# Performance work log

Measured on AMD Instinct MI355X. Metric: run time of the kernel, lower is better.

## Reference

```python
import jax, jax.numpy as jnp
import numpy as np

B, V, J, NB = 1024, 3889, 33, 10
P = (J - 1) * 9  # 288 pose-blendshape basis


def setup_inputs() -> dict:
    key = jax.random.key(0)
    ks = jax.random.split(key, 9)
    n = lambda k, s, sc=1.0: jax.random.normal(k, s, dtype=jnp.float32) * sc
    betas = n(ks[0], (B, NB))
    global_orient = n(ks[1], (B, 3), 0.5)
    body_pose = n(ks[2], (B, (J - 1) * 3), 0.3)
    transl = n(ks[3], (B, 3))
    v_template = n(ks[4], (V, 3))
    shapedirs = n(ks[5], (V, 3, NB), 0.01)
    posedirs = n(ks[6], (P, V * 3), 0.01)
    jr = jax.random.uniform(ks[7], (J, V), dtype=jnp.float32)
    J_regressor = jr / jnp.sum(jr, axis=1, keepdims=True)  # rows sum to 1
    w = jax.random.uniform(ks[8], (V, J), dtype=jnp.float32)
    lbs_weights = w / jnp.sum(w, axis=1, keepdims=True)
    # kinematic tree: chain, parents[i] < i; root parent handled specially
    parents = np.maximum(np.arange(J) - 1, 0).astype(np.int64)
    return {"betas": betas, "global_orient": global_orient, "body_pose": body_pose,
            "transl": transl, "v_template": v_template, "shapedirs": shapedirs,
            "posedirs": posedirs, "J_regressor": J_regressor,
            "lbs_weights": lbs_weights, "parents": parents}


def _rodrigues(rot_vecs):
    """Axis-angle [.., 3] -> rotation matrices [.., 3, 3] (Rodrigues)."""
    angle = jnp.linalg.norm(rot_vecs + 1e-8, axis=-1, keepdims=True)
    axis = rot_vecs / angle
    rx, ry, rz = axis[..., 0], axis[..., 1], axis[..., 2]
    z = jnp.zeros_like(rx)
    K = jnp.stack([z, -rz, ry, rz, z, -rx, -ry, rx, z], axis=-1)
    K = K.reshape(rot_vecs.shape[:-1] + (3, 3))
    s = jnp.sin(angle)[..., None]
    c = jnp.cos(angle)[..., None]
    return jnp.eye(3, dtype=rot_vecs.dtype) + s * K + (1.0 - c) * (K @ K)


def _lbs(betas, global_orient, body_pose, transl, v_template, shapedirs,
         posedirs, J_regressor, lbs_weights, parents):
    Bn = betas.shape[0]
    par = np.asarray(parents)  # static kinematic tree
    Jn = par.shape[0]
    # shape blendshapes
    v_shaped = v_template[None] + jnp.einsum('bl,vcl->bvc', betas, shapedirs)
    joints = jnp.einsum('jv,bvc->bjc', J_regressor, v_shaped)  # [B,J,3]
    # pose -> rotation matrices
    full_pose = jnp.concatenate([global_orient, body_pose], axis=1).reshape(Bn, Jn, 3)
    rot = _rodrigues(full_pose)  # [B,J,3,3]
    # pose blendshapes (identity-subtracted, root excluded)
    pose_feat = (rot[:, 1:] - jnp.eye(3, dtype=rot.dtype)).reshape(Bn, -1)  # [B,288]
    v_posed = v_shaped + (pose_feat @ posedirs).reshape(Bn, -1, 3)
    # forward kinematics: compose 4x4 transforms along the tree
    rel = joints.at[:, 1:].add(-joints[:, par[1:]])  # relative joint locations
    Tmat = jnp.concatenate([rot, rel[..., None]], axis=-1)  # [B,J,3,4]
    bottom = jnp.broadcast_to(jnp.array([0., 0., 0., 1.], Tmat.dtype), (Bn, Jn, 1, 4))
    Tmat = jnp.concatenate([Tmat, bottom], axis=2)  # [B,J,4,4]
    chain = [Tmat[:, 0]]
    for i in range(1, Jn):  # fixed small loop over joints
        chain.append(chain[int(par[i])] @ Tmat[:, i])
    transforms = jnp.stack(chain, axis=1)  # [B,J,4,4]
    # remove rest-pose joint locations from the transforms
    jh = jnp.concatenate([joints, jnp.zeros((Bn, Jn, 1), joints.dtype)], axis=-1)[..., None]
    A = transforms - jnp.pad(transforms @ jh, ((0, 0), (0, 0), (0, 0), (3, 0)))
    # linear blend skinning
    T = jnp.einsum('vj,bjmn->bvmn', lbs_weights, A)  # [B,V,4,4]
    vh = jnp.concatenate([v_posed, jnp.ones(v_posed.shape[:-1] + (1,), v_posed.dtype)], axis=-1)
    verts = jnp.einsum('bvmn,bvn->bvm', T, vh)[..., :3]
    return verts + transl[:, None]


def reference(betas, global_orient, body_pose, transl, v_template, shapedirs,
              posedirs, J_regressor, lbs_weights, parents):
    return _lbs(betas, global_orient, body_pose, transl, v_template, shapedirs,
                posedirs, J_regressor, lbs_weights, parents)
```

## Files before the change

### kernel.cpp

```cpp
#include <hip/hip_runtime.h>
#include <math.h>

#define B_  1024
#define V_  3889
#define J_  33
#define NB_ 10
#define P_  288
#define N3  11667
#define NT_ 122
#define NPAD (NT_*96)

typedef short bf16x8 __attribute__((ext_vector_type(8)));
typedef float f32x4  __attribute__((ext_vector_type(4)));

__device__ __forceinline__ unsigned short f2bf(float f) {
  union { float f; unsigned u; } v; v.f = f;
  unsigned r = v.u + 0x7FFFu + ((v.u >> 16) & 1u);
  return (unsigned short)(r >> 16);
}
__device__ __forceinline__ float bf2f(unsigned short h) {
  union { unsigned u; float f; } v; v.u = ((unsigned)h) << 16; return v.f;
}

#define PREP_JS   33
#define PREP_CVT  399
#define PREP_NB   463

__global__ __launch_bounds__(256) void k_prep(
    const float* __restrict__ Jreg, const float* __restrict__ vt,
    const float* __restrict__ sd, const float* __restrict__ pdirs,
    const float* __restrict__ lbsw,
    float* __restrict__ JS, float* __restrict__ bj,
    unsigned short* __restrict__ pdT, unsigned short* __restrict__ wbf)
{
  __shared__ __align__(16) unsigned char su[38016];
  const int bid = blockIdx.x;
  const int t = threadIdx.x;

  if (bid < PREP_JS) {
    float* red = (float*)su;
    const int j = bid;
    if (t < 128) {
      float acc[33];
      #pragma unroll
      for (int e = 0; e < 33; ++e) acc[e] = 0.f;
      for (int v = t; v < V_; v += 128) {
        float r = Jreg[j*V_ + v];
        #pragma unroll
        for (int c = 0; c < 3; ++c) {
          acc[c*11 + 10] += r * vt[v*3 + c];
          #pragma unroll
          for (int l = 0; l < NB_; ++l)
            acc[c*11 + l] += r * sd[v*30 + c*10 + l];
        }
      }
      #pragma unroll
      for (int e = 0; e < 33; ++e) red[e*128 + t] = acc[e];
    }
    __syncthreads();
    if (t < 33) {
      float s = 0.f;
      for (int i = 0; i < 128; ++i) s += red[t*128 + i];
      int c = t / 11, l = t % 11;
      if (l == 10) bj[j*3 + c] = s;
      else         JS[(j*3 + c)*NB_ + l] = s;
    }
  } else if (bid < PREP_CVT) {
    float* tile = (float*)su;
    const int bb = bid - PREP_JS;
    const int nt = bb / 3;
    const int c0 = (bb % 3) * 32;
    for (int i = t; i < P_*32; i += 256) {
      int k = i >> 5, c = i & 31;
      int gc = nt*96 + c0 + c;
      tile[k*33 + c] = (gc < N3) ? pdirs[(size_t)k*N3 + gc] : 0.f;
    }
    __syncthreads();
    for (int o = t; o < 32*P_; o += 256) {
      int c = o / P_, k = o % P_;
      pdT[((size_t)(nt*96 + c0 + c))*P_ + k] = f2bf(tile[k*33 + c]);
    }
  } else {
    const int bb = bid - PREP_CVT;
    const int total = 4096*96;
    for (int i = bb*256 + t; i < total; i += 64*256) {
      int v = i / 96, k = i - 96*v;
      float val = 0.f;
      if (v < V_) {
        if (k < 33) val = lbsw[(size_t)v*33 + k];
        else if (k < 66) {
          float w = lbsw[(size_t)v*33 + (k-33)];
          val = w - bf2f(f2bf(w));
        }
      }
      wbf[i] = f2bf(val);
    }
  }
}

__global__ __launch_bounds__(64) void k_pose(
    const float* __restrict__ betas, const float* __restrict__ go,
    const float* __restrict__ bp, const float* __restrict__ JS,
    const float* __restrict__ bj,
    unsigned short* __restrict__ pfb,
    unsigned short* __restrict__ Abf)
{
  const int b = blockIdx.x;
  const int t = threadIdx.x;
  __shared__ float rot[J_][9];
  __shared__ float jnt[J_][3];
  __shared__ float Ash[J_][12];
  __shared__ float bsh[NB_];
  if (t < NB_) bsh[t] = betas[b*NB_ + t];
  __syncthreads();
  if (t < J_) {
    #pragma unroll
    for (int c = 0; c < 3; ++c) {
      float s = bj[t*3 + c];
      #pragma unroll
      for (int l = 0; l < NB_; ++l) s += bsh[l] * JS[(t*3 + c)*NB_ + l];
      jnt[t][c] = s;
    }
    float px, py, pz;
    if (t == 0) { px = go[b*3+0]; py = go[b*3+1]; pz = go[b*3+2]; }
    else {
      const float* p = bp + (size_t)b*((J_-1)*3) + (t-1)*3;
      px = p[0]; py = p[1]; pz = p[2];
    }
    float ax = px + 1e-8f, ay = py + 1e-8f, az = pz + 1e-8f;
    float ang = sqrtf(ax*ax + ay*ay + az*az);
    float inv = 1.0f / ang;
    float ux = px*inv, uy = py*inv, uz = pz*inv;
    float sn = sinf(ang), cs = cosf(ang);
    float K[9] = {0.f,-uz,uy,  uz,0.f,-ux,  -uy,ux,0.f};
    float R[9];
    #pragma unroll
    for (int r = 0; r < 3; ++r)
      #pragma unroll
      for (int c = 0; c < 3; ++c) {
        float k2 = K[r*3+0]*K[0*3+c] + K[r*3+1]*K[1*3+c] + K[r*3+2]*K[2*3+c];
        float id = (r == c) ? 1.f : 0.f;
        R[r*3+c] = id + sn*K[r*3+c] + (1.f - cs)*k2;
      }
    #pragma unroll
    for (int e = 0; e < 9; ++e) rot[t][e] = R[e];
    if (t >= 1) {
      #pragma unroll
      for (int e = 0; e < 9; ++e)
        pfb[(size_t)b*P_ + (t-1)*9 + e] = f2bf(R[e] - ((e==0||e==4||e==8) ? 1.f : 0.f));
    }
  }
  __syncthreads();
  if (t == 0) {
    float G[12];
    #pragma unroll
    for (int r = 0; r < 3; ++r) {
      G[r*4+0] = rot[0][r*3+0]; G[r*4+1] = rot[0][r*3+1];
      G[r*4+2] = rot[0][r*3+2]; G[r*4+3] = jnt[0][r];
    }
    for (int j = 0; j < J_; ++j) {
      if (j > 0) {
        float rel0 = jnt[j][0] - jnt[j-1][0];
        float rel1 = jnt[j][1] - jnt[j-1][1];
        float rel2 = jnt[j][2] - jnt[j-1][2];
        float N[12];
        #pragma unroll
        for (int r = 0; r < 3; ++r) {
          #pragma unroll
          for (int c = 0; c < 3; ++c)
            N[r*4+c] = G[r*4+0]*rot[j][0*3+c] + G[r*4+1]*rot[j][1*3+c] + G[r*4+2]*rot[j][2*3+c];
          N[r*4+3] = G[r*4+0]*rel0 + G[r*4+1]*rel1 + G[r*4+2]*rel2 + G[r*4+3];
        }
        #pragma unroll
        for (int e = 0; e < 12; ++e) G[e] = N[e];
      }
      #pragma unroll
      for (int r = 0; r < 3; ++r) {
        Ash[j][r*4+0] = G[r*4+0];
        Ash[j][r*4+1] = G[r*4+1];
        Ash[j][r*4+2] = G[r*4+2];
        Ash[j][r*4+3] = G[r*4+3] - (G[r*4+0]*jnt[j][0] + G[r*4+1]*jnt[j][1] + G[r*4+2]*jnt[j][2]);
      }
    }
  }
  __syncthreads();
  const float* Af = &Ash[0][0];
  for (int i = t; i < 1536; i += 64) {
    int n = i / 96, k = i - 96*n;
    int j = (k < 33) ? k : ((k < 66) ? (k - 33) : -1);
    float val = 0.f;
    if (j >= 0) {
      if (n < 12) val = Af[j*12 + n];
      else if (n < 15) {
        float tr = Af[j*12 + (n-12)*4 + 3];
        val = tr - bf2f(f2bf(tr));
      }
    }
    Abf[(size_t)b*1536 + i] = f2bf(val);
  }
}

#define TS 17

__global__ __launch_bounds__(256, 2) void k_gs(
    const float* __restrict__ betas,
    const float* __restrict__ vt, const float* __restrict__ sd,
    const unsigned short* __restrict__ pdT,
    const unsigned short* __restrict__ pfb_g,
    const float* __restrict__ transl,
    const unsigned short* __restrict__ wbf,
    const unsigned short* __restrict__ Abf,
    float* __restrict__ out)
{
  __shared__ float s_beta[640];
  __shared__ float s_tr[192];
  __shared__ float s_vp[64*100];
  __shared__ float s_T[4][2*32*TS];

  const int tid = threadIdx.x;
  const int nt = blockIdx.x, bt = blockIdx.y;
  const int b0 = bt*64;
  const int lane = tid & 63, wid = tid >> 6;
  const int wm = wid >> 1, wn = wid & 1;
  const int l15 = lane & 15, lg = lane >> 4;

  for (int i = tid; i < 64*NB_; i += 256) s_beta[i] = betas[(size_t)b0*NB_ + i];
  for (int i = tid; i < 192; i += 256) s_tr[i] = transl[(size_t)b0*3 + i];

  bf16x8 afr[2][3];
  #pragma unroll
  for (int mt = 0; mt < 2; ++mt) {
    const int vrow = nt*32 + mt*16 + l15;
    #pragma unroll
    for (int ks = 0; ks < 3; ++ks)
      afr[mt][ks] = *(const bf16x8*)&wbf[(size_t)vrow*96 + ks*32 + lg*8];
  }
  __syncthreads();

  f32x4 acc[2][3];
  #pragma unroll
  for (int f = 0; f < 3; ++f) {
    int colL = wn*48 + f*16 + l15;
    int gc = nt*96 + colL;
    if (gc < N3) {
      int v = gc/3, c = gc - 3*v;
      float base = vt[gc];
      float sval[2][4];
      #pragma unroll
      for (int mi = 0; mi < 2; ++mi)
        #pragma unroll
        for (int reg = 0; reg < 4; ++reg) sval[mi][reg] = base;
      #pragma unroll
      for (int l = 0; l < NB_; ++l) {
        float sdv = sd[(size_t)v*30 + c*10 + l];
        #pragma unroll
        for (int mi = 0; mi < 2; ++mi) {
          int row_b = mi*32 + wm*16 + lg*4;
          #pragma unroll
          for (int reg = 0; reg < 4; ++reg)
            sval[mi][reg] += s_beta[(row_b+reg)*NB_ + l] * sdv;
        }
      }
      #pragma unroll
      for (int mi = 0; mi < 2; ++mi) {
        acc[mi][f][0]=sval[mi][0]; acc[mi][f][1]=sval[mi][1];
        acc[mi][f][2]=sval[mi][2]; acc[mi][f][3]=sval[mi][3];
      }
    } else {
      #pragma unroll
      for (int mi = 0; mi < 2; ++mi)
        acc[mi][f] = (f32x4){0.f,0.f,0.f,0.f};
    }
  }

  const unsigned short* __restrict__ pfrow0 =
      pfb_g + (size_t)(b0 + wm*16 + l15)*P_ + lg*8;
  const unsigned short* __restrict__ pfrow1 =
      pfb_g + (size_t)(b0 + 32 + wm*16 + l15)*P_ + lg*8;
  const unsigned short* __restrict__ pdrow =
      pdT + (size_t)(nt*96 + wn*48 + l15)*P_ + lg*8;
  #pragma unroll
  for (int ks = 0; ks < 9; ++ks) {
    bf16x8 a0 = *(const bf16x8*)(pfrow0 + ks*32);
    bf16x8 a1 = *(const bf16x8*)(pfrow1 + ks*32);
    #pragma unroll
    for (int f = 0; f < 3; ++f) {
      bf16x8 b = *(const bf16x8*)(pdrow + (size_t)f*16*P_ + ks*32);
      acc[0][f] = __builtin_amdgcn_mfma_f32_16x16x32_bf16(a0, b, acc[0][f], 0, 0, 0);
      acc[1][f] = __builtin_amdgcn_mfma_f32_16x16x32_bf16(a1, b, acc[1][f], 0, 0, 0);
    }
  }

  bf16x8 bcur[2][3];
  #pragma unroll
  for (int h = 0; h < 2; ++h) {
    const unsigned short* Ab = Abf + (size_t)(b0 + wid*16 + h)*1536;
    #pragma unroll
    for (int ks = 0; ks < 3; ++ks)
      bcur[h][ks] = *(const bf16x8*)&Ab[l15*96 + ks*32 + lg*8];
  }

  #pragma unroll
  for (int f = 0; f < 3; ++f) {
    int colL = wn*48 + f*16 + l15;
    #pragma unroll
    for (int mi = 0; mi < 2; ++mi) {
      int row_b = mi*32 + wm*16 + lg*4;
      #pragma unroll
      for (int reg = 0; reg < 4; ++reg)
        s_vp[(row_b+reg)*100 + colL] = acc[mi][f][reg];
    }
  }
  __syncthreads();

  float* Tw = &s_T[wid][0];
  const int h2 = lane >> 5, vl = lane & 31;
  const int v = nt*32 + vl;

  float pxc = s_vp[(wid*16 + h2)*100 + vl*3 + 0];
  float pyc = s_vp[(wid*16 + h2)*100 + vl*3 + 1];
  float pzc = s_vp[(wid*16 + h2)*100 + vl*3 + 2];

  #pragma unroll 2
  for (int g = 0; g < 8; ++g) {
    bf16x8 bnxt[2][3];
    float pxn = 0.f, pyn = 0.f, pzn = 0.f;
    if (g < 7) {
      #pragma unroll
      for (int h = 0; h < 2; ++h) {
        const unsigned short* Ab = Abf + (size_t)(b0 + wid*16 + (g+1)*2 + h)*1536;
        #pragma unroll
        for (int ks = 0; ks < 3; ++ks)
          bnxt[h][ks] = *(const bf16x8*)&Ab[l15*96 + ks*32 + lg*8];
      }
      int bln = wid*16 + (g+1)*2 + h2;
      pxn = s_vp[bln*100 + vl*3 + 0];
      pyn = s_vp[bln*100 + vl*3 + 1];
      pzn = s_vp[bln*100 + vl*3 + 2];
    }

    #pragma unroll
    for (int h = 0; h < 2; ++h) {
      f32x4 t0 = {0.f,0.f,0.f,0.f}, t1 = t0;
      #pragma unroll
      for (int ks = 0; ks < 3; ++ks) {
        t0 = __builtin_amdgcn_mfma_f32_16x16x32_bf16(afr[0][ks], bcur[h][ks], t0, 0, 0, 0);
        t1 = __builtin_amdgcn_mfma_f32_16x16x32_bf16(afr[1][ks], bcur[h][ks], t1, 0, 0, 0);
      }
      #pragma unroll
      for (int reg = 0; reg < 4; ++reg) {
        Tw[h*32*TS + (lg*4+reg)*TS + l15]      = t0[reg];
        Tw[h*32*TS + (16+lg*4+reg)*TS + l15]   = t1[reg];
      }
    }
    {
      const int bl2 = wid*16 + g*2 + h2;
      const int b2  = b0 + bl2;
      const float* Tr = Tw + h2*32*TS + vl*TS;
      float o0 = Tr[0]*pxc + Tr[1]*pyc + Tr[2]*pzc  + Tr[3]  + Tr[12] + s_tr[bl2*3+0];
      float o1 = Tr[4]*pxc + Tr[5]*pyc + Tr[6]*pzc  + Tr[7]  + Tr[13] + s_tr[bl2*3+1];
      float o2 = Tr[8]*pxc + Tr[9]*pyc + Tr[10]*pzc + Tr[11] + Tr[14] + s_tr[bl2*3+2];
      if (v < V_) {
        size_t po = (size_t)b2*N3 + (size_t)v*3;
        out[po+0] = o0; out[po+1] = o1; out[po+2] = o2;
      }
    }
    if (g < 7) {
      #pragma unroll
      for (int h = 0; h < 2; ++h)
        #pragma unroll
        for (int ks = 0; ks < 3; ++ks)
          bcur[h][ks] = bnxt[h][ks];
      pxc = pxn; pyc = pyn; pzc = pzn;
    }
  }
}

extern "C" void kernel_launch(void* const* d_in, const int* in_sizes, int n_in,
                              void* d_out, int out_size, void* d_ws, size_t ws_size,
                              hipStream_t stream) {
  const float* betas  = (const float*)d_in[0];
  const float* go     = (const float*)d_in[1];
  const float* bp     = (const float*)d_in[2];
  const float* transl = (const float*)d_in[3];
  const float* vt     = (const float*)d_in[4];
  const float* sd     = (const float*)d_in[5];
  const float* pdirs  = (const float*)d_in[6];
  const float* Jreg   = (const float*)d_in[7];
  const float* lbsw   = (const float*)d_in[8];
  float* out = (float*)d_out;
  char* wb = (char*)d_ws;

  float* JS            = (float*)(wb + 0);
  float* bj            = (float*)(wb + 4096);
  unsigned short* pfb  = (unsigned short*)(wb + 1630720);
  unsigned short* Abf  = (unsigned short*)(wb + 2221056);
  unsigned short* pdT  = (unsigned short*)(wb + 5366784);
  unsigned short* wbf  = (unsigned short*)(wb + 12112896);

  hipLaunchKernelGGL(k_prep, dim3(PREP_NB), dim3(256), 0, stream,
                     Jreg, vt, sd, pdirs, lbsw, JS, bj, pdT, wbf);
  hipLaunchKernelGGL(k_pose, dim3(B_), dim3(64), 0, stream,
                     betas, go, bp, JS, bj, pfb, Abf);
  hipLaunchKernelGGL(k_gs,   dim3(NT_, B_/64), dim3(256), 0, stream,
                     betas, vt, sd, pdT, pfb, transl, wbf, Abf, out);
}
```

Baseline: 105.5 us.

## Fold shape blendshapes and template into the pose MFMA GEMM as extra K columns

Extends the pose-blendshape GEMM from K=288 to K=320. The added columns hold betas and a constant 1 on the activation side, and shapedirs and v_template on the weight side. The scalar FP32 shape-blend loop, the betas shared-memory staging and one syncthreads in the main kernel are removed, and that work runs as one extra MFMA k-step. Shapedirs and v_template are now applied in bf16 instead of fp32, which may cost accuracy, especially on the template offset.

```diff
diff --git a/kernel.cpp b/kernel.cpp
--- a/kernel.cpp
+++ b/kernel.cpp
@@ -6,6 +6,7 @@
 #define J_  33
 #define NB_ 10
 #define P_  288
+#define K2  320
 #define N3  11667
 #define NT_ 122
 #define NPAD (NT_*96)
@@ -78,7 +79,18 @@
     __syncthreads();
     for (int o = t; o < 32*P_; o += 256) {
       int c = o / P_, k = o % P_;
-      pdT[((size_t)(nt*96 + c0 + c))*P_ + k] = f2bf(tile[k*33 + c]);
+      pdT[((size_t)(nt*96 + c0 + c))*K2 + k] = f2bf(tile[k*33 + c]);
+    }
+    for (int o = t; o < 32*32; o += 256) {
+      int c = o >> 5, e = o & 31;
+      int gc = nt*96 + c0 + c;
+      float val = 0.f;
+      if (gc < N3) {
+        int v = gc/3, ch = gc - 3*v;
+        if (e < NB_)       val = sd[(size_t)v*30 + ch*10 + e];
+        else if (e == NB_) val = vt[gc];
+      }
+      pdT[((size_t)(nt*96 + c0 + c))*K2 + P_ + e] = f2bf(val);
     }
   } else {
     const int bb = bid - PREP_CVT;
@@ -147,8 +159,12 @@
     if (t >= 1) {
       #pragma unroll
       for (int e = 0; e < 9; ++e)
-        pfb[(size_t)b*P_ + (t-1)*9 + e] = f2bf(R[e] - ((e==0||e==4||e==8) ? 1.f : 0.f));
-    }
+        pfb[(size_t)b*K2 + (t-1)*9 + e] = f2bf(R[e] - ((e==0||e==4||e==8) ? 1.f : 0.f));
+    }
+  }
+  if (t < 32) {
+    float val = (t < NB_) ? bsh[t] : ((t == NB_) ? 1.0f : 0.f);
+    pfb[(size_t)b*K2 + P_ + t] = f2bf(val);
   }
   __syncthreads();
   if (t == 0) {
@@ -203,8 +219,6 @@
 #define TS 17
 
 __global__ __launch_bounds__(256, 2) void k_gs(
-    const float* __restrict__ betas,
-    const float* __restrict__ vt, const float* __restrict__ sd,
     const unsigned short* __restrict__ pdT,
     const unsigned short* __restrict__ pfb_g,
     const float* __restrict__ transl,
@@ -212,7 +226,6 @@
     const unsigned short* __restrict__ Abf,
     float* __restrict__ out)
 {
-  __shared__ float s_beta[640];
   __shared__ float s_tr[192];
   __shared__ float s_vp[64*100];
   __shared__ float s_T[4][2*32*TS];
@@ -224,7 +237,6 @@
   const int wm = wid >> 1, wn = wid & 1;
   const int l15 = lane & 15, lg = lane >> 4;
 
-  for (int i = tid; i < 64*NB_; i += 256) s_beta[i] = betas[(size_t)b0*NB_ + i];
   for (int i = tid; i < 192; i += 256) s_tr[i] = transl[(size_t)b0*3 + i];
 
   bf16x8 afr[2][3];
@@ -235,57 +247,27 @@
     for (int ks = 0; ks < 3; ++ks)
       afr[mt][ks] = *(const bf16x8*)&wbf[(size_t)vrow*96 + ks*32 + lg*8];
   }
-  __syncthreads();
 
   f32x4 acc[2][3];
   #pragma unroll
-  for (int f = 0; f < 3; ++f) {
-    int colL = wn*48 + f*16 + l15;
-    int gc = nt*96 + colL;
-    if (gc < N3) {
-      int v = gc/3, c = gc - 3*v;
-      float base = vt[gc];
-      float sval[2][4];
-      #pragma unroll
-      for (int mi = 0; mi < 2; ++mi)
-        #pragma unroll
-        for (int reg = 0; reg < 4; ++reg) sval[mi][reg] = base;
-      #pragma unroll
-      for (int l = 0; l < NB_; ++l) {
-        float sdv = sd[(size_t)v*30 + c*10 + l];
-        #pragma unroll
-        for (int mi = 0; mi < 2; ++mi) {
-          int row_b = mi*32 + wm*16 + lg*4;
-          #pragma unroll
-          for (int reg = 0; reg < 4; ++reg)
-            sval[mi][reg] += s_beta[(row_b+reg)*NB_ + l] * sdv;
-        }
-      }
-      #pragma unroll
-      for (int mi = 0; mi < 2; ++mi) {
-        acc[mi][f][0]=sval[mi][0]; acc[mi][f][1]=sval[mi][1];
-        acc[mi][f][2]=sval[mi][2]; acc[mi][f][3]=sval[mi][3];
-      }
-    } else {
-      #pragma unroll
-      for (int mi = 0; mi < 2; ++mi)
-        acc[mi][f] = (f32x4){0.f,0.f,0.f,0.f};
-    }
-  }
+  for (int mi = 0; mi < 2; ++mi)
+    #pragma unroll
+    for (int f = 0; f < 3; ++f)
+      acc[mi][f] = (f32x4){0.f,0.f,0.f,0.f};
 
   const unsigned short* __restrict__ pfrow0 =
-      pfb_g + (size_t)(b0 + wm*16 + l15)*P_ + lg*8;
+      pfb_g + (size_t)(b0 + wm*16 + l15)*K2 + lg*8;
   const unsigned short* __restrict__ pfrow1 =
-      pfb_g + (size_t)(b0 + 32 + wm*16 + l15)*P_ + lg*8;
+      pfb_g + (size_t)(b0 + 32 + wm*16 + l15)*K2 + lg*8;
   const unsigned short* __restrict__ pdrow =
-      pdT + (size_t)(nt*96 + wn*48 + l15)*P_ + lg*8;
-  #pragma unroll
-  for (int ks = 0; ks < 9; ++ks) {
+      pdT + (size_t)(nt*96 + wn*48 + l15)*K2 + lg*8;
+  #pragma unroll
+  for (int ks = 0; ks < 10; ++ks) {
     bf16x8 a0 = *(const bf16x8*)(pfrow0 + ks*32);
     bf16x8 a1 = *(const bf16x8*)(pfrow1 + ks*32);
     #pragma unroll
     for (int f = 0; f < 3; ++f) {
-      bf16x8 b = *(const bf16x8*)(pdrow + (size_t)f*16*P_ + ks*32);
+      bf16x8 b = *(const bf16x8*)(pdrow + (size_t)f*16*K2 + ks*32);
       acc[0][f] = __builtin_amdgcn_mfma_f32_16x16x32_bf16(a0, b, acc[0][f], 0, 0, 0);
       acc[1][f] = __builtin_amdgcn_mfma_f32_16x16x32_bf16(a1, b, acc[1][f], 0, 0, 0);
     }
@@ -393,15 +375,15 @@
 
   float* JS            = (float*)(wb + 0);
   float* bj            = (float*)(wb + 4096);
-  unsigned short* pfb  = (unsigned short*)(wb + 1630720);
-  unsigned short* Abf  = (unsigned short*)(wb + 2221056);
-  unsigned short* pdT  = (unsigned short*)(wb + 5366784);
-  unsigned short* wbf  = (unsigned short*)(wb + 12112896);
+  unsigned short* pfb  = (unsigned short*)(wb + 8192);
+  unsigned short* Abf  = (unsigned short*)(wb + 663552);
+  unsigned short* pdT  = (unsigned short*)(wb + 3809280);
+  unsigned short* wbf  = (unsigned short*)(wb + 11304960);
 
   hipLaunchKernelGGL(k_prep, dim3(PREP_NB), dim3(256), 0, stream,
                      Jreg, vt, sd, pdirs, lbsw, JS, bj, pdT, wbf);
   hipLaunchKernelGGL(k_pose, dim3(B_), dim3(64), 0, stream,
                      betas, go, bp, JS, bj, pfb, Abf);
   hipLaunchKernelGGL(k_gs,   dim3(NT_, B_/64), dim3(256), 0, stream,
-                     betas, vt, sd, pdT, pfb, transl, wbf, Abf, out);
-}
+                     pdT, pfb, transl, wbf, Abf, out);
+}
```

After: 118.1 us. +12.0%, slower.
